# Performance work log

Hardware: AMD Instinct MI355X
Metric: run time of the kernel (lower is better)

## Reference

```python
import jax, jax.numpy as jnp
import numpy as np
import math

INPUT_SIZE = 20
HIDDEN = 1500
OUTPUT = 20
MLP_HID = math.ceil(5 / 4 * HIDDEN)  # 1875
T = 4096


def setup_inputs() -> dict:
    key = jax.random.key(0)
    ks = jax.random.split(key, 10)
    s_lstm = 1.0 / np.sqrt(HIDDEN)
    s1 = 1.0 / np.sqrt(HIDDEN)
    s2 = 1.0 / np.sqrt(MLP_HID)
    return {
        "input_seq": jax.random.normal(ks[0], (T, INPUT_SIZE), dtype=jnp.float32),
        "W_ih": jax.random.uniform(ks[1], (4 * HIDDEN, INPUT_SIZE), jnp.float32, -s_lstm, s_lstm),
        "W_hh": jax.random.uniform(ks[2], (4 * HIDDEN, HIDDEN), jnp.float32, -s_lstm, s_lstm),
        "b_ih": jax.random.uniform(ks[3], (4 * HIDDEN,), jnp.float32, -s_lstm, s_lstm),
        "b_hh": jax.random.uniform(ks[4], (4 * HIDDEN,), jnp.float32, -s_lstm, s_lstm),
        "W1": jax.random.uniform(ks[5], (MLP_HID, HIDDEN), jnp.float32, -s1, s1),
        "b1": jax.random.uniform(ks[6], (MLP_HID,), jnp.float32, -s1, s1),
        "W2": jax.random.uniform(ks[7], (OUTPUT, MLP_HID), jnp.float32, -s2, s2),
        "b2": jax.random.uniform(ks[8], (OUTPUT,), jnp.float32, -s2, s2),
    }


def reference(input_seq, W_ih, W_hh, b_ih, b_hh, W1, b1, W2, b2):
    H = W_hh.shape[1]
    # Precompute input contribution for all timesteps: (T, 4H)
    x_proj = input_seq @ W_ih.T + (b_ih + b_hh)

    def step(carry, xp):
        h, c = carry
        gates = xp + h @ W_hh.T  # (4H,)
        i, f, g, o = jnp.split(gates, 4)
        i = jax.nn.sigmoid(i)
        f = jax.nn.sigmoid(f)
        g = jnp.tanh(g)
        o = jax.nn.sigmoid(o)
        c_new = f * c + i * g
        h_new = o * jnp.tanh(c_new)
        return (h_new, c_new), None

    h0 = jnp.zeros((H,), dtype=input_seq.dtype)
    c0 = jnp.zeros((H,), dtype=input_seq.dtype)
    (h_last, _), _ = jax.lax.scan(step, (h0, c0), x_proj)
    # Dropout is identity in eval mode. Module returns predictions[-1],
    # which only depends on the last hidden state.
    hid = h_last @ W1.T + b1
    return hid @ W2.T + b2
```

## Files before the change

### kernel.cpp

```cpp
#include <hip/hip_runtime.h>
#include <math.h>

#define TT 4096
#define HH 1500
#define NB 125
#define NT 512
#define NREP 8

typedef unsigned uv4 __attribute__((ext_vector_type(4)));
typedef _Float16 h2f __attribute__((ext_vector_type(2)));
typedef _Float16 h4f __attribute__((ext_vector_type(4)));

#define ALD4(p)   __hip_atomic_load((p), __ATOMIC_RELAXED, __HIP_MEMORY_SCOPE_AGENT)
#define AST4(p,v) __hip_atomic_store((p), (v), __ATOMIC_RELAXED, __HIP_MEMORY_SCOPE_AGENT)
#define AST8(p,v) __hip_atomic_store((p), (v), __ATOMIC_RELAXED, __HIP_MEMORY_SCOPE_AGENT)

__device__ __forceinline__ float fast_sigmoid(float z) {
  return 1.0f / (1.0f + __expf(-z));
}
__device__ __forceinline__ float fast_tanh(float z) {
  float az = fabsf(z);
  float e  = __expf(-2.0f * az);
  float r  = (1.0f - e) / (1.0f + e);
  return copysignf(r, z);
}
__device__ __forceinline__ float dot2(unsigned wb, unsigned hb, float acc) {
#if __has_builtin(__builtin_amdgcn_fdot2)
  return __builtin_amdgcn_fdot2(__builtin_bit_cast(h2f, wb),
                                __builtin_bit_cast(h2f, hb), acc, false);
#else
  h2f w = __builtin_bit_cast(h2f, wb), h = __builtin_bit_cast(h2f, hb);
  acc = fmaf((float)w.x, (float)h.x, acc);
  return fmaf((float)w.y, (float)h.y, acc);
#endif
}

__device__ __forceinline__ void poll3(const unsigned* a0, const unsigned* a1,
                                      const unsigned* a2,
                                      uv4& v0, uv4& v1, uv4& v2) {
  asm volatile(
      "global_load_dwordx4 %0, %3, off sc0 sc1\n\t"
      "global_load_dwordx4 %1, %4, off sc0 sc1\n\t"
      "global_load_dwordx4 %2, %5, off sc0 sc1\n\t"
      "s_waitcnt vmcnt(0)"
      : "=&v"(v0), "=&v"(v1), "=&v"(v2)
      : "v"(a0), "v"(a1), "v"(a2)
      : "memory");
}
__device__ __forceinline__ h4f cvt4h(uv4 v) {
  h4f r;
  r.x = (_Float16)__uint_as_float(v.x);
  r.y = (_Float16)__uint_as_float(v.y);
  r.z = (_Float16)__uint_as_float(v.z);
  r.w = (_Float16)__uint_as_float(v.w);
  return r;
}

__global__
__attribute__((amdgpu_flat_work_group_size(NT, NT), amdgpu_waves_per_eu(2, 2)))
void lstm_fused(
    const float* __restrict__ x,
    const float* __restrict__ Wih,
    const float* __restrict__ Whh,
    const float* __restrict__ bih,
    const float* __restrict__ bhh,
    const float* __restrict__ W1,
    const float* __restrict__ b1,
    const float* __restrict__ W2,
    const float* __restrict__ b2,
    float* __restrict__ out,
    unsigned* __restrict__ ws)
{
  const int tid = threadIdx.x;
  const int bid = blockIdx.x;
  const int wv  = tid >> 6;
  const int ln  = tid & 63;

  unsigned* pub  = ws;
  unsigned* hidp = ws + NREP * 2 * 1536;

  __shared__ __align__(16) _Float16 lds_wh[48 * 1536];
  __shared__ __align__(16) _Float16 lds_hh[1536];
  __shared__ __align__(16) float    lds_hf[1536];
  __shared__ float lds_xp[2][48];
  __shared__ float lds_gs[4][12];
  float* lds_hd = (float*)lds_wh;

  for (int hi = tid; hi < 48 * 1536; hi += NT) {
    const int r = hi / 1536, k = hi - r * 1536;
    const int u = r >> 2, g = r & 3;
    const size_t grow = (size_t)(g * HH + bid * 12 + u) * HH;
    const float v = (k < HH) ? Whh[grow + k] : 0.f;
    lds_wh[hi] = (_Float16)v;
  }

  const int uu = (wv < 6) ? wv : 0;
  const uv4* wpA = ((const uv4*)lds_wh) + (size_t)(2 * uu) * 4 * 192;
  const uv4* wpB = wpA + 4 * 192;
  const uv4* hp = (const uv4*)lds_hh;

  float4 wx0, wx1, wx2, wx3, wx4;
  float4 xr0, xr1, xr2, xr3, xr4;
  float bias = 0.f;
  if (wv == 6 && ln < 48) {
    const int g = ln / 12, u = ln - g * 12;
    const int row = g * HH + bid * 12 + u;
    const float4* sp = (const float4*)(Wih + row * 20);
    wx0 = sp[0]; wx1 = sp[1]; wx2 = sp[2]; wx3 = sp[3]; wx4 = sp[4];
    bias = bih[row] + bhh[row];
    const float4* xx = (const float4*)x;
    xr0 = xx[0]; xr1 = xx[1]; xr2 = xx[2]; xr3 = xx[3]; xr4 = xx[4];
  }

  float c = 0.f;

  if (tid < 12 * NREP)
    AST4(pub + (tid / 12) * 3072 + 12 * bid + (tid % 12), 1u);

  __syncthreads();

  unsigned* myrep = pub + (bid & (NREP - 1)) * 3072;

  for (int t = 0; t < TT; ++t) {
    const int s = t & 1;
    const unsigned tag = (unsigned)((t + 1) & 15);

    uv4 pw[24];
    if (wv < 6) {
      #pragma unroll
      for (int g = 0; g < 4; ++g) {
        #pragma unroll
        for (int m = 0; m < 3; ++m) {
          pw[g * 3 + m]      = wpA[g * 192 + ln + 64 * m];
          pw[12 + g * 3 + m] = wpB[g * 192 + ln + 64 * m];
        }
      }
    } else {
      if (wv == 6 && ln < 48) {
        float sx = bias;
        sx += wx0.x*xr0.x + wx0.y*xr0.y + wx0.z*xr0.z + wx0.w*xr0.w;
        sx += wx1.x*xr1.x + wx1.y*xr1.y + wx1.z*xr1.z + wx1.w*xr1.w;
        sx += wx2.x*xr2.x + wx2.y*xr2.y + wx2.z*xr2.z + wx2.w*xr2.w;
        sx += wx3.x*xr3.x + wx3.y*xr3.y + wx3.z*xr3.z + wx3.w*xr3.w;
        sx += wx4.x*xr4.x + wx4.y*xr4.y + wx4.z*xr4.z + wx4.w*xr4.w;
        lds_xp[s][ln] = sx;
      }
      const int p4 = (tid - 384) << 2;
      unsigned* base = myrep + s * 1536;
      uv4 v0, v1, v2;
      for (;;) {
        poll3(base + p4, base + p4 + 512, base + p4 + 1024, v0, v1, v2);
        unsigned miss = ((v0.x & 15u) ^ tag) | ((v0.y & 15u) ^ tag)
                      | ((v0.z & 15u) ^ tag) | ((v0.w & 15u) ^ tag)
                      | ((v1.x & 15u) ^ tag) | ((v1.y & 15u) ^ tag)
                      | ((v1.z & 15u) ^ tag) | ((v1.w & 15u) ^ tag);
        if (p4 + 1024 < HH)
          miss |= ((v2.x & 15u) ^ tag) | ((v2.y & 15u) ^ tag)
                | ((v2.z & 15u) ^ tag) | ((v2.w & 15u) ^ tag);
        if (!__any(miss != 0u)) break;
        __builtin_amdgcn_s_sleep(1);
      }
      *(h4f*)(lds_hh + p4)       = cvt4h(v0);
      *(h4f*)(lds_hh + p4 + 512) = cvt4h(v1);
      h4f z = {(_Float16)0.f, (_Float16)0.f, (_Float16)0.f, (_Float16)0.f};
      *(h4f*)(lds_hh + p4 + 1024) = (p4 + 1024 < HH) ? cvt4h(v2) : z;
    }
    __syncthreads();

    if (wv < 6) {
      uv4 hv[3];
      #pragma unroll
      for (int m = 0; m < 3; ++m) hv[m] = hp[ln + 64 * m];
      float a0[4] = {0.f, 0.f, 0.f, 0.f};
      float a1[4] = {0.f, 0.f, 0.f, 0.f};
      #pragma unroll
      for (int g = 0; g < 4; ++g) {
        #pragma unroll
        for (int m = 0; m < 3; ++m) {
          const uv4 h = hv[m];
          const uv4 qa = pw[g * 3 + m];
          a0[g] = dot2(qa.x, h.x, a0[g]);
          a0[g] = dot2(qa.y, h.y, a0[g]);
          a0[g] = dot2(qa.z, h.z, a0[g]);
          a0[g] = dot2(qa.w, h.w, a0[g]);
          const uv4 qb = pw[12 + g * 3 + m];
          a1[g] = dot2(qb.x, h.x, a1[g]);
          a1[g] = dot2(qb.y, h.y, a1[g]);
          a1[g] = dot2(qb.z, h.z, a1[g]);
          a1[g] = dot2(qb.w, h.w, a1[g]);
        }
      }
      #pragma unroll
      for (int g = 0; g < 4; ++g) {
        a0[g] += __shfl_xor(a0[g], 16, 64);
        a0[g] += __shfl_xor(a0[g], 32, 64);
        a1[g] += __shfl_xor(a1[g], 16, 64);
        a1[g] += __shfl_xor(a1[g], 32, 64);
      }
      const int q4 = ln >> 4;
      float v0 = (q4 == 0) ? a0[0] : (q4 == 1) ? a0[1] : (q4 == 2) ? a0[2] : a0[3];
      float v1 = (q4 == 0) ? a1[0] : (q4 == 1) ? a1[1] : (q4 == 2) ? a1[2] : a1[3];
      #pragma unroll
      for (int off = 1; off <= 8; off <<= 1) {
        v0 += __shfl_xor(v0, off, 64);
        v1 += __shfl_xor(v1, off, 64);
      }
      if ((ln & 15) == 0) {
        lds_gs[q4][2 * wv]     = v0;
        lds_gs[q4][2 * wv + 1] = v1;
      }
    } else if (wv == 6 && ln < 48 && (t + 1) < TT) {
      const float4* xx = (const float4*)(x + 20 * (t + 1));
      xr0 = xx[0]; xr1 = xx[1]; xr2 = xx[2]; xr3 = xx[3]; xr4 = xx[4];
    }
    __syncthreads();

    if (wv == 7) {
      unsigned bits = 0u;
      if (ln < 12) {
        const int u = ln;
        const float zi = lds_gs[0][u] + lds_xp[s][0 + u];
        const float zf = lds_gs[1][u] + lds_xp[s][12 + u];
        const float zg = lds_gs[2][u] + lds_xp[s][24 + u];
        const float zo = lds_gs[3][u] + lds_xp[s][36 + u];
        const float ig = fast_sigmoid(zi);
        const float fg = fast_sigmoid(zf);
        const float gg = fast_tanh(zg);
        const float og = fast_sigmoid(zo);
        c = fg * c + ig * gg;
        const float hn = og * fast_tanh(c);
        bits = (__float_as_uint(hn) & ~15u) | (unsigned)((t + 2) & 15);
      }
      const int m6 = ln % 6;
      const unsigned d0 = (unsigned)__shfl((int)bits, 2 * m6, 64);
      const unsigned d1 = (unsigned)__shfl((int)bits, 2 * m6 + 1, 64);
      if (ln < 48) {
        const int rep = ln / 6;
        const unsigned long long dd =
            (unsigned long long)d0 | ((unsigned long long)d1 << 32);
        AST8((unsigned long long*)(pub + rep * 3072 + ((t + 1) & 1) * 1536 +
                                   12 * bid + 2 * m6), dd);
      }
    }
  }

  {
    const unsigned tagf = (unsigned)((TT + 1) & 15);
    if (tid < 375) {
      const unsigned* ap = myrep + (tid << 2);
      uv4 v;
      for (;;) {
        asm volatile("global_load_dwordx4 %0, %1, off sc0 sc1\n\t"
                     "s_waitcnt vmcnt(0)"
                     : "=&v"(v) : "v"(ap) : "memory");
        const unsigned miss = ((v.x & 15u) ^ tagf) | ((v.y & 15u) ^ tagf)
                            | ((v.z & 15u) ^ tagf) | ((v.w & 15u) ^ tagf);
        if (!miss) break;
        __builtin_amdgcn_s_sleep(1);
      }
      float4 f = {__uint_as_float(v.x), __uint_as_float(v.y),
                  __uint_as_float(v.z), __uint_as_float(v.w)};
      *(float4*)(lds_hf + (tid << 2)) = f;
    } else if (tid < 384) {
      float4 z4 = {0.f, 0.f, 0.f, 0.f};
      *(float4*)(lds_hf + (tid << 2)) = z4;
    }
  }
  __syncthreads();

  {
    const float4* h4 = (const float4*)lds_hf;
    for (int k = wv; k < 15; k += 8) {
      const int r = bid + NB * k;
      const float4* wrow = (const float4*)(W1 + (size_t)r * HH);
      float ss = 0.f;
      #pragma unroll
      for (int m = 0; m < 6; ++m) {
        const int idx = ln + 64 * m;
        if (idx < 375) {
          const float4 a = wrow[idx], hv = h4[idx];
          ss += a.x*hv.x + a.y*hv.y + a.z*hv.z + a.w*hv.w;
        }
      }
      #pragma unroll
      for (int off = 32; off > 0; off >>= 1) ss += __shfl_xor(ss, off, 64);
      if (ln == 0) {
        const float vv = ss + b1[r];
        AST4(hidp + r, (__float_as_uint(vv) & ~15u) | 5u);
      }
    }
  }
  if (bid != 0) return;

  __syncthreads();
  for (int j = tid; j < 1875; j += NT) {
    unsigned bts;
    for (;;) {
      bts = ALD4(hidp + j);
      if ((bts & 15u) == 5u) break;
      __builtin_amdgcn_s_sleep(1);
    }
    lds_hd[j] = __uint_as_float(bts);
  }
  __syncthreads();

  for (int r = wv; r < 20; r += 8) {
    float ss = 0.f;
    for (int k = ln; k < 1875; k += 64)
      ss = fmaf(W2[(size_t)r * 1875 + k], lds_hd[k], ss);
    #pragma unroll
    for (int off = 32; off > 0; off >>= 1) ss += __shfl_xor(ss, off, 64);
    if (ln == 0) out[r] = ss + b2[r];
  }
}

extern "C" void kernel_launch(void* const* d_in, const int* in_sizes, int n_in,
                              void* d_out, int out_size, void* d_ws, size_t ws_size,
                              hipStream_t stream) {
  const float* x   = (const float*)d_in[0];
  const float* Wih = (const float*)d_in[1];
  const float* Whh = (const float*)d_in[2];
  const float* bih = (const float*)d_in[3];
  const float* bhh = (const float*)d_in[4];
  const float* W1  = (const float*)d_in[5];
  const float* b1  = (const float*)d_in[6];
  const float* W2  = (const float*)d_in[7];
  const float* b2  = (const float*)d_in[8];
  float* out   = (float*)d_out;
  unsigned* ws = (unsigned*)d_ws;

  hipLaunchKernelGGL(lstm_fused, dim3(NB), dim3(NT), 0, stream,
                     x, Wih, Whh, bih, bhh, W1, b1, W2, b2, out, ws);
}
```

Baseline: 10.25 ms.

## Split h-vector polling across compute waves and drop one block barrier per step

Each of the six compute waves now polls and converts its own 256-element slice of the published hidden state. It then dots that slice against all 48 gate rows held in registers, one row per lane, using a swizzled LDS weight layout. Per-wave partial sums go to a double-buffered LDS array and are reduced by the gate-update wave. This removes the dedicated polling waves, the first __syncthreads, and the cross-lane shuffle reductions. In exchange, each lane carries 32 uv4 registers, 16 lanes per wave sit idle in the dot product, and there are more concurrent polling waves per block.

After: 10.47 ms. 2.1% more time.

```diff
diff --git a/kernel.cpp b/kernel.cpp
--- a/kernel.cpp
+++ b/kernel.cpp
@@ -35,18 +35,6 @@
 #endif
 }
 
-__device__ __forceinline__ void poll3(const unsigned* a0, const unsigned* a1,
-                                      const unsigned* a2,
-                                      uv4& v0, uv4& v1, uv4& v2) {
-  asm volatile(
-      "global_load_dwordx4 %0, %3, off sc0 sc1\n\t"
-      "global_load_dwordx4 %1, %4, off sc0 sc1\n\t"
-      "global_load_dwordx4 %2, %5, off sc0 sc1\n\t"
-      "s_waitcnt vmcnt(0)"
-      : "=&v"(v0), "=&v"(v1), "=&v"(v2)
-      : "v"(a0), "v"(a1), "v"(a2)
-      : "memory");
-}
 __device__ __forceinline__ h4f cvt4h(uv4 v) {
   h4f r;
   r.x = (_Float16)__uint_as_float(v.x);
@@ -80,24 +68,25 @@
   unsigned* hidp = ws + NREP * 2 * 1536;
 
   __shared__ __align__(16) _Float16 lds_wh[48 * 1536];
-  __shared__ __align__(16) _Float16 lds_hh[1536];
+  __shared__ __align__(16) _Float16 lds_hs[6][256];
   __shared__ __align__(16) float    lds_hf[1536];
   __shared__ float lds_xp[2][48];
-  __shared__ float lds_gs[4][12];
+  __shared__ float lds_ps[2][6][48];
   float* lds_hd = (float*)lds_wh;
 
   for (int hi = tid; hi < 48 * 1536; hi += NT) {
     const int r = hi / 1536, k = hi - r * 1536;
     const int u = r >> 2, g = r & 3;
-    const size_t grow = (size_t)(g * HH + bid * 12 + u) * HH;
-    const float v = (k < HH) ? Whh[grow + k] : 0.f;
-    lds_wh[hi] = (_Float16)v;
-  }
-
-  const int uu = (wv < 6) ? wv : 0;
-  const uv4* wpA = ((const uv4*)lds_wh) + (size_t)(2 * uu) * 4 * 192;
-  const uv4* wpB = wpA + 4 * 192;
-  const uv4* hp = (const uv4*)lds_hh;
+    const float v = (k < HH) ? Whh[(size_t)(g * HH + bid * 12 + u) * HH + k]
+                             : 0.f;
+    const int w = k >> 8, o = k & 255, cch = o >> 3, j = o & 7;
+    const int cs = cch ^ (r & 31);
+    lds_wh[r * 1536 + w * 256 + cs * 8 + j] = (_Float16)v;
+  }
+  if (wv == 5 && ln >= 55) {
+    h4f z = {(_Float16)0.f, (_Float16)0.f, (_Float16)0.f, (_Float16)0.f};
+    *(h4f*)(lds_hs[5] + 4 * ln) = z;
+  }
 
   float4 wx0, wx1, wx2, wx3, wx4;
   float4 xr0, xr1, xr2, xr3, xr4;
@@ -121,22 +110,52 @@
 
   unsigned* myrep = pub + (bid & (NREP - 1)) * 3072;
 
+  const int q    = (wv << 6) | ln;
+  const int live = (q < 375);
+  const int qc   = live ? q : 0;
+  const _Float16* wr = lds_wh + ln * 1536 + (wv << 8);
+
   for (int t = 0; t < TT; ++t) {
     const int s = t & 1;
     const unsigned tag = (unsigned)((t + 1) & 15);
 
-    uv4 pw[24];
     if (wv < 6) {
-      #pragma unroll
-      for (int g = 0; g < 4; ++g) {
+      uv4 pw[32];
+      if (ln < 48) {
         #pragma unroll
-        for (int m = 0; m < 3; ++m) {
-          pw[g * 3 + m]      = wpA[g * 192 + ln + 64 * m];
-          pw[12 + g * 3 + m] = wpB[g * 192 + ln + 64 * m];
-        }
-      }
-    } else {
-      if (wv == 6 && ln < 48) {
+        for (int cc = 0; cc < 32; ++cc)
+          pw[cc] = *(const uv4*)(wr + ((cc ^ (ln & 31)) << 3));
+      }
+      const unsigned* ap = myrep + s * 1536 + (qc << 2);
+      uv4 v;
+      for (;;) {
+        asm volatile("global_load_dwordx4 %0, %1, off sc0 sc1\n\t"
+                     "s_waitcnt vmcnt(0)"
+                     : "=&v"(v) : "v"(ap) : "memory");
+        unsigned miss = 0u;
+        if (live)
+          miss = ((v.x & 15u) ^ tag) | ((v.y & 15u) ^ tag)
+               | ((v.z & 15u) ^ tag) | ((v.w & 15u) ^ tag);
+        if (!__any(miss != 0u)) break;
+        __builtin_amdgcn_s_sleep(1);
+      }
+      if (live) *(h4f*)(lds_hs[wv] + 4 * ln) = cvt4h(v);
+      if (ln < 48) {
+        const uv4* hsl = (const uv4*)lds_hs[wv];
+        float ps = 0.f;
+        #pragma unroll
+        for (int cc = 0; cc < 32; ++cc) {
+          const uv4 hq = hsl[cc];
+          const uv4 wq = pw[cc];
+          ps = dot2(wq.x, hq.x, ps);
+          ps = dot2(wq.y, hq.y, ps);
+          ps = dot2(wq.z, hq.z, ps);
+          ps = dot2(wq.w, hq.w, ps);
+        }
+        lds_ps[s][wv][ln] = ps;
+      }
+    } else if (wv == 6) {
+      if (ln < 48) {
         float sx = bias;
         sx += wx0.x*xr0.x + wx0.y*xr0.y + wx0.z*xr0.z + wx0.w*xr0.w;
         sx += wx1.x*xr1.x + wx1.y*xr1.y + wx1.z*xr1.z + wx1.w*xr1.w;
@@ -144,85 +163,27 @@
         sx += wx3.x*xr3.x + wx3.y*xr3.y + wx3.z*xr3.z + wx3.w*xr3.w;
         sx += wx4.x*xr4.x + wx4.y*xr4.y + wx4.z*xr4.z + wx4.w*xr4.w;
         lds_xp[s][ln] = sx;
-      }
-      const int p4 = (tid - 384) << 2;
-      unsigned* base = myrep + s * 1536;
-      uv4 v0, v1, v2;
-      for (;;) {
-        poll3(base + p4, base + p4 + 512, base + p4 + 1024, v0, v1, v2);
-        unsigned miss = ((v0.x & 15u) ^ tag) | ((v0.y & 15u) ^ tag)
-                      | ((v0.z & 15u) ^ tag) | ((v0.w & 15u) ^ tag)
-                      | ((v1.x & 15u) ^ tag) | ((v1.y & 15u) ^ tag)
-                      | ((v1.z & 15u) ^ tag) | ((v1.w & 15u) ^ tag);
-        if (p4 + 1024 < HH)
-          miss |= ((v2.x & 15u) ^ tag) | ((v2.y & 15u) ^ tag)
-                | ((v2.z & 15u) ^ tag) | ((v2.w & 15u) ^ tag);
-        if (!__any(miss != 0u)) break;
-        __builtin_amdgcn_s_sleep(1);
-      }
-      *(h4f*)(lds_hh + p4)       = cvt4h(v0);
-      *(h4f*)(lds_hh + p4 + 512) = cvt4h(v1);
-      h4f z = {(_Float16)0.f, (_Float16)0.f, (_Float16)0.f, (_Float16)0.f};
-      *(h4f*)(lds_hh + p4 + 1024) = (p4 + 1024 < HH) ? cvt4h(v2) : z;
-    }
-    __syncthreads();
-
-    if (wv < 6) {
-      uv4 hv[3];
-      #pragma unroll
-      for (int m = 0; m < 3; ++m) hv[m] = hp[ln + 64 * m];
-      float a0[4] = {0.f, 0.f, 0.f, 0.f};
-      float a1[4] = {0.f, 0.f, 0.f, 0.f};
-      #pragma unroll
-      for (int g = 0; g < 4; ++g) {
-        #pragma unroll
-        for (int m = 0; m < 3; ++m) {
-          const uv4 h = hv[m];
-          const uv4 qa = pw[g * 3 + m];
-          a0[g] = dot2(qa.x, h.x, a0[g]);
-          a0[g] = dot2(qa.y, h.y, a0[g]);
-          a0[g] = dot2(qa.z, h.z, a0[g]);
-          a0[g] = dot2(qa.w, h.w, a0[g]);
-          const uv4 qb = pw[12 + g * 3 + m];
-          a1[g] = dot2(qb.x, h.x, a1[g]);
-          a1[g] = dot2(qb.y, h.y, a1[g]);
-          a1[g] = dot2(qb.z, h.z, a1[g]);
-          a1[g] = dot2(qb.w, h.w, a1[g]);
-        }
-      }
-      #pragma unroll
-      for (int g = 0; g < 4; ++g) {
-        a0[g] += __shfl_xor(a0[g], 16, 64);
-        a0[g] += __shfl_xor(a0[g], 32, 64);
-        a1[g] += __shfl_xor(a1[g], 16, 64);
-        a1[g] += __shfl_xor(a1[g], 32, 64);
-      }
-      const int q4 = ln >> 4;
-      float v0 = (q4 == 0) ? a0[0] : (q4 == 1) ? a0[1] : (q4 == 2) ? a0[2] : a0[3];
-      float v1 = (q4 == 0) ? a1[0] : (q4 == 1) ? a1[1] : (q4 == 2) ? a1[2] : a1[3];
-      #pragma unroll
-      for (int off = 1; off <= 8; off <<= 1) {
-        v0 += __shfl_xor(v0, off, 64);
-        v1 += __shfl_xor(v1, off, 64);
-      }
-      if ((ln & 15) == 0) {
-        lds_gs[q4][2 * wv]     = v0;
-        lds_gs[q4][2 * wv + 1] = v1;
-      }
-    } else if (wv == 6 && ln < 48 && (t + 1) < TT) {
-      const float4* xx = (const float4*)(x + 20 * (t + 1));
-      xr0 = xx[0]; xr1 = xx[1]; xr2 = xx[2]; xr3 = xx[3]; xr4 = xx[4];
+        if (t + 1 < TT) {
+          const float4* xx = (const float4*)(x + 20 * (t + 1));
+          xr0 = xx[0]; xr1 = xx[1]; xr2 = xx[2]; xr3 = xx[3]; xr4 = xx[4];
+        }
+      }
     }
     __syncthreads();
 
     if (wv == 7) {
       unsigned bits = 0u;
       if (ln < 12) {
-        const int u = ln;
-        const float zi = lds_gs[0][u] + lds_xp[s][0 + u];
-        const float zf = lds_gs[1][u] + lds_xp[s][12 + u];
-        const float zg = lds_gs[2][u] + lds_xp[s][24 + u];
-        const float zo = lds_gs[3][u] + lds_xp[s][36 + u];
+        float4 a = {0.f, 0.f, 0.f, 0.f};
+        #pragma unroll
+        for (int w = 0; w < 6; ++w) {
+          const float4 p = *(const float4*)&lds_ps[s][w][ln << 2];
+          a.x += p.x; a.y += p.y; a.z += p.z; a.w += p.w;
+        }
+        const float zi = a.x + lds_xp[s][0 + ln];
+        const float zf = a.y + lds_xp[s][12 + ln];
+        const float zg = a.z + lds_xp[s][24 + ln];
+        const float zo = a.w + lds_xp[s][36 + ln];
         const float ig = fast_sigmoid(zi);
         const float fg = fast_sigmoid(zf);
         const float gg = fast_tanh(zg);
```
